# Kernel optimization log

Hardware: AMD Instinct MI355X
Metric: run time of the kernel (lower is better)

The kernel has to match this reference:

```python
import jax, jax.numpy as jnp
import numpy as np

DIM = 1024
HEADS = 16
HEAD_DIM = DIM // HEADS
EPS = 1e-5
THETA = 10000.0


def _rope(t):
    # t: (b, s, d). lucidrains rotary: interleaved pairs, full-dim rotation, theta=10000.
    b, s, d = t.shape
    inv_freq = 1.0 / (THETA ** (jnp.arange(0, d, 2, dtype=jnp.float32) / d))  # (d/2,)
    ang = jnp.arange(s, dtype=jnp.float32)[:, None] * inv_freq[None, :]        # (s, d/2)
    cos, sin = jnp.cos(ang), jnp.sin(ang)
    tp = t.reshape(b, s, d // 2, 2)
    x1, x2 = tp[..., 0], tp[..., 1]
    o1 = x1 * cos - x2 * sin
    o2 = x2 * cos + x1 * sin
    return jnp.stack([o1, o2], axis=-1).reshape(b, s, d)


def setup_inputs() -> dict:
    key = jax.random.key(0)
    ks = jax.random.split(key, 10)
    b, s, d = 2, 2048, DIM
    scale = 1.0 / np.sqrt(d)
    return {
        "x": jax.random.normal(ks[0], (b, s, d), dtype=jnp.float32),
        "mask": jax.random.normal(ks[1], (b, s, s), dtype=jnp.float32),
        "ln_g": jnp.ones((d,), dtype=jnp.float32),
        "ln_b": jnp.zeros((d,), dtype=jnp.float32),
        "w_qkv": jax.random.normal(ks[2], (3 * d, d), dtype=jnp.float32) * scale,
        "b_qkv": jnp.zeros((3 * d,), dtype=jnp.float32),
        "in_w": jax.random.normal(ks[3], (3 * d, d), dtype=jnp.float32) * scale,
        "in_b": jnp.zeros((3 * d,), dtype=jnp.float32),
        "out_w": jax.random.normal(ks[4], (d, d), dtype=jnp.float32) * scale,
        "out_b": jnp.zeros((d,), dtype=jnp.float32),
    }


def reference(x, mask, ln_g, ln_b, w_qkv, b_qkv, in_w, in_b, out_w, out_b):
    b, s, d = x.shape
    # LayerNorm
    mu = jnp.mean(x, axis=-1, keepdims=True)
    var = jnp.mean((x - mu) ** 2, axis=-1, keepdims=True)
    xn = (x - mu) * jax.lax.rsqrt(var + EPS) * ln_g + ln_b
    # fused qkv projection, then chunk
    qkv = xn @ w_qkv.T + b_qkv
    q, k, v = jnp.split(qkv, 3, axis=-1)
    # RoPE on q, k (full dim, interleaved pairs)
    q = _rope(q)
    k = _rope(k)
    # nn.MultiheadAttention re-applies its own in-projection
    wq, wk, wv = jnp.split(in_w, 3, axis=0)
    bq, bk, bv = jnp.split(in_b, 3, axis=0)
    def to_heads(t, w, bias):
        t = t @ w.T + bias
        return t.reshape(b, s, HEADS, HEAD_DIM).transpose(0, 2, 1, 3)  # (b,h,s,hd)
    qh = to_heads(q, wq, bq)
    kh = to_heads(k, wk, bk)
    vh = to_heads(v, wv, bv)
    scores = jnp.einsum('bhid,bhjd->bhij', qh, kh) / np.sqrt(HEAD_DIM)
    scores = scores + mask[:, None, :, :]  # mask repeated over heads
    attn = jax.nn.softmax(scores, axis=-1)
    out = jnp.einsum('bhij,bhjd->bhid', attn, vh)
    out = out.transpose(0, 2, 1, 3).reshape(b, s, d)
    return out @ out_w.T + out_b
```

## Files before the change

### kernel.cpp

```cpp
#include <hip/hip_runtime.h>

using u16 = unsigned short;
using u32 = unsigned int;
typedef __attribute__((ext_vector_type(8))) short short8;
typedef __attribute__((ext_vector_type(4))) float f32x4;

#define LOG2E 1.4426950408889634f
#define SCALE2 0.18033688011112042f

__device__ __forceinline__ u16 f2b(float f) {
  union { float f; unsigned u; } v; v.f = f;
  unsigned r = v.u + 0x7fffu + ((v.u >> 16) & 1u);
  return (u16)(r >> 16);
}

__device__ __forceinline__ void wg_barrier() {
  asm volatile("s_waitcnt lgkmcnt(0)\n\ts_barrier" ::: "memory");
}

__device__ __forceinline__ void gload_lds16(const void* g, void* l) {
  __builtin_amdgcn_global_load_lds(
      (const __attribute__((address_space(1))) unsigned int*)g,
      (__attribute__((address_space(3))) unsigned int*)l, 16, 0, 0);
}

__global__ __launch_bounds__(256) void prep(const float* __restrict__ w_qkv, u16* __restrict__ wqkv_b,
                                            const float* __restrict__ in_w, u16* __restrict__ inw_b,
                                            const float* __restrict__ out_w, u16* __restrict__ outw_b,
                                            float2* __restrict__ rtab,
                                            const float* __restrict__ mask, u16* __restrict__ maskp,
                                            const float* __restrict__ x,
                                            const float* __restrict__ ln_g,
                                            const float* __restrict__ ln_b,
                                            u16* __restrict__ xn) {
  __shared__ u16 T[128 * 68];
  __shared__ float sbuf[4], ssbuf[4];
  int blk = blockIdx.x, t = threadIdx.x;
  if (blk < 7168) {
    int i = blk * 256 + t;
    const float* s; u16* d; int off;
    if (i < 786432)       { s = w_qkv; d = wqkv_b; off = i; }
    else if (i < 1572864) { s = in_w;  d = inw_b;  off = i - 786432; }
    else                  { s = out_w; d = outw_b; off = i - 1572864; }
    float4 v = ((const float4*)s)[off];
    uint2 o;
    o.x = (unsigned)f2b(v.x) | ((unsigned)f2b(v.y) << 16);
    o.y = (unsigned)f2b(v.z) | ((unsigned)f2b(v.w) << 16);
    ((uint2*)d)[off] = o;
  } else if (blk < 11264) {
    int idx = (blk - 7168) * 256 + t;
    int pos = idx >> 9, i = idx & 511;
    float ifreq = exp2f(-(float)(2 * i) * (13.287712379549449f / 1024.0f));
    float ang = (float)pos * ifreq;
    rtab[idx] = make_float2(__cosf(ang), __sinf(ang));
  } else if (blk < 12288) {
    int mb = blk - 11264;
    int kt = mb & 31, qt = (mb >> 5) & 15, bb = mb >> 9;
    const float* src = mask + ((size_t)bb * 2048 + qt * 128) * 2048 + kt * 64;
    #pragma unroll
    for (int it = 0; it < 8; it++) {
      int id = it * 256 + t;
      int r = id >> 4, c4 = (id & 15) * 4;
      float4 v = *(const float4*)(src + (size_t)r * 2048 + c4);
      T[r * 68 + c4 + 0] = f2b(v.x * LOG2E);
      T[r * 68 + c4 + 1] = f2b(v.y * LOG2E);
      T[r * 68 + c4 + 2] = f2b(v.z * LOG2E);
      T[r * 68 + c4 + 3] = f2b(v.w * LOG2E);
    }
    __syncthreads();
    size_t obase = (size_t)(((bb * 16 + qt) * 32) + kt) * 8192;
    #pragma unroll
    for (int it = 0; it < 2; it++) {
      int pos = it * 256 + t;
      int l15 = pos & 15, g = pos >> 4;
      int w = g >> 3, p = (g >> 2) & 1, qd = g & 3;
      int qlocal = w * 32 + p * 16 + l15;
      u16 vals[16];
      #pragma unroll
      for (int mt = 0; mt < 4; mt++)
        #pragma unroll
        for (int reg = 0; reg < 4; reg++)
          vals[mt * 4 + reg] = T[qlocal * 68 + mt * 16 + qd * 4 + reg];
      uint4* dst = (uint4*)(maskp + obase + (size_t)pos * 16);
      dst[0] = *(uint4*)&vals[0];
      dst[1] = *(uint4*)&vals[8];
    }
  } else {
    int row = blk - 12288;
    const float* xr = x + (size_t)row * 1024;
    float4 v = *(const float4*)(xr + t * 4);
    float s = v.x + v.y + v.z + v.w;
    float ss = v.x * v.x + v.y * v.y + v.z * v.z + v.w * v.w;
    #pragma unroll
    for (int m = 1; m < 64; m <<= 1) {
      s  += __shfl_xor(s, m);
      ss += __shfl_xor(ss, m);
    }
    int wave = t >> 6, lane = t & 63;
    if (lane == 0) { sbuf[wave] = s; ssbuf[wave] = ss; }
    __syncthreads();
    s  = sbuf[0] + sbuf[1] + sbuf[2] + sbuf[3];
    ss = ssbuf[0] + ssbuf[1] + ssbuf[2] + ssbuf[3];
    float mean = s * (1.0f / 1024.0f);
    float var  = ss * (1.0f / 1024.0f) - mean * mean;
    float rstd = 1.0f / sqrtf(var + 1e-5f);
    float4 gv = *(const float4*)(ln_g + t * 4);
    float4 bv = *(const float4*)(ln_b + t * 4);
    uint2 o;
    o.x = (unsigned)f2b((v.x - mean) * rstd * gv.x + bv.x) |
          ((unsigned)f2b((v.y - mean) * rstd * gv.y + bv.y) << 16);
    o.y = (unsigned)f2b((v.z - mean) * rstd * gv.z + bv.z) |
          ((unsigned)f2b((v.w - mean) * rstd * gv.w + bv.w) << 16);
    *(uint2*)(xn + (size_t)row * 1024 + t * 4) = o;
  }
}

template<bool SLAB, bool OUT_BF16, bool ROPE, bool WVT>
__global__ __launch_bounds__(256, 3) void gemm_pipe(const u16* __restrict__ A, int lda,
                                                    const u16* __restrict__ W,
                                                    const float* __restrict__ bias,
                                                    const float2* __restrict__ rtab,
                                                    float* __restrict__ Cf,
                                                    u16* __restrict__ Cb,
                                                    u16* __restrict__ vT,
                                                    int ldc, int K) {
  __shared__ u16 As[3][128 * 32];
  __shared__ u16 Bs[3][128 * 32];
  int n0 = blockIdx.x * 128, m0 = blockIdx.y * 128;
  int aoff = SLAB ? ((n0 >> 10) << 10) : 0;
  int tid = threadIdx.x;
  int lane = tid & 63, l15 = lane & 15, quad = lane >> 4;
  int w = tid >> 6, mw = w & 1, nw = w >> 1;
  const u16* Abase = A + (size_t)m0 * lda + aoff;
  const u16* Wbase = W + (size_t)n0 * K;
  f32x4 acc[4][4];
  #pragma unroll
  for (int i = 0; i < 4; i++)
    #pragma unroll
    for (int j = 0; j < 4; j++) acc[i][j] = (f32x4){0.f, 0.f, 0.f, 0.f};

  int rl = lane >> 2;
  int qs = ((lane & 3) ^ ((lane >> 3) & 3)) * 16;
  const char* gA0 = (const char*)(Abase + (size_t)(w * 16 + rl) * lda) + qs;
  const char* gA1 = (const char*)(Abase + (size_t)((w + 4) * 16 + rl) * lda) + qs;
  const char* gB0 = (const char*)(Wbase + (size_t)(w * 16 + rl) * K) + qs;
  const char* gB1 = (const char*)(Wbase + (size_t)((w + 4) * 16 + rl) * K) + qs;
  int p16 = (quad ^ ((l15 >> 1) & 3)) * 8;

  #define ISSUE(bf)                                                           \
    gload_lds16(gA0, &As[bf][(w) * 512]);                                     \
    gload_lds16(gA1, &As[bf][(w + 4) * 512]);                                 \
    gload_lds16(gB0, &Bs[bf][(w) * 512]);                                     \
    gload_lds16(gB1, &Bs[bf][(w + 4) * 512]);                                 \
    gA0 += 64; gA1 += 64; gB0 += 64; gB1 += 64;
  #define WBAR4() asm volatile("s_waitcnt vmcnt(4) lgkmcnt(0)\n\ts_barrier" ::: "memory")
  #define WBAR0() asm volatile("s_waitcnt vmcnt(0) lgkmcnt(0)\n\ts_barrier" ::: "memory")
  #define COMPUTE(bf)                                                         \
    {                                                                         \
      short8 af[4], bfr[4];                                                   \
      _Pragma("unroll")                                                       \
      for (int mt = 0; mt < 4; mt++)                                          \
        af[mt] = *(const short8*)&As[bf][(mw * 64 + mt * 16 + l15) * 32 + p16]; \
      _Pragma("unroll")                                                       \
      for (int nt = 0; nt < 4; nt++)                                          \
        bfr[nt] = *(const short8*)&Bs[bf][(nw * 64 + nt * 16 + l15) * 32 + p16]; \
      _Pragma("unroll")                                                       \
      for (int mt = 0; mt < 4; mt++)                                          \
        _Pragma("unroll")                                                     \
        for (int nt = 0; nt < 4; nt++)                                        \
          acc[mt][nt] = __builtin_amdgcn_mfma_f32_16x16x32_bf16(              \
              af[mt], bfr[nt], acc[mt][nt], 0, 0, 0);                         \
    }

  ISSUE(0);
  ISSUE(1);
  WBAR4();
  #pragma unroll 1
  for (int tt = 0; tt < 10; ++tt) {
    ISSUE(2); COMPUTE(0); WBAR4();
    ISSUE(0); COMPUTE(1); WBAR4();
    ISSUE(1); COMPUTE(2); WBAR4();
  }
  COMPUTE(0); WBAR0();
  COMPUTE(1);
  #undef ISSUE
  #undef WBAR4
  #undef WBAR0
  #undef COMPUTE

  int mb = m0 + mw * 64, nb = n0 + nw * 64;
  float bv[4];
  #pragma unroll
  for (int nt = 0; nt < 4; nt++) bv[nt] = bias[nb + nt * 16 + l15];
  #pragma unroll
  for (int mt = 0; mt < 4; mt++)
    #pragma unroll
    for (int nt = 0; nt < 4; nt++) {
      int col = nb + nt * 16 + l15;
      if (WVT && col >= 2048) {
        int hh = (col - 2048) >> 6, dd = (col - 2048) & 63;
        int row0 = mb + mt * 16 + quad * 4;
        int bbi = row0 >> 11, s0 = row0 & 2047;
        u16 vv[4];
        #pragma unroll
        for (int reg = 0; reg < 4; reg++) vv[reg] = f2b(acc[mt][nt][reg] + bv[nt]);
        *(uint2*)&vT[((size_t)((bbi * 16 + hh) * 64 + dd)) * 2048 + s0] = *(uint2*)vv;
      } else {
        #pragma unroll
        for (int reg = 0; reg < 4; reg++) {
          int row = mb + mt * 16 + quad * 4 + reg;
          float val = acc[mt][nt][reg] + bv[nt];
          if (ROPE && col < 2048) {
            float pr = __shfl_xor(val, 1);
            float2 cs = rtab[(size_t)(row & 2047) * 512 + ((col & 1023) >> 1)];
            val = (col & 1) ? fmaf(val, cs.x, pr * cs.y)
                            : fmaf(val, cs.x, -pr * cs.y);
          }
          if (OUT_BF16) Cb[(size_t)row * ldc + col] = f2b(val);
          else          Cf[(size_t)row * ldc + col] = val;
        }
      }
    }
}

__global__ __launch_bounds__(512, 4) void attn_mfma(const u16* __restrict__ qkv2,
                                                    const u16* __restrict__ vT,
                                                    const u16* __restrict__ maskp,
                                                    u16* __restrict__ attn_out) {
  __shared__ u16 Kb[2][64 * 72];
  __shared__ u16 Vb[2][64 * 72];
  __shared__ u16 Ps[128 * 72];
  __shared__ float lsf[128];
  int h = blockIdx.x, qt = blockIdx.y, bb = blockIdx.z;
  int tid = threadIdx.x;
  int lane = tid & 63, l15 = lane & 15, quad = lane >> 4;
  int w = tid >> 6;
  int wq = w & 3, wk = w >> 2;
  int sr = tid >> 3, sc = (tid & 7) * 8;
  const u16* kslab = qkv2 + ((size_t)bb * 2048) * 3072 + 1024 + h * 64;
  const u16* vslab = vT + ((size_t)((bb * 16 + h) * 64)) * 2048;

  {
    int r = tid >> 2, c0 = (tid & 3) * 16;
    const u16* src = qkv2 + (size_t)(bb * 2048 + qt * 128 + r) * 3072 + h * 64 + c0;
    *(uint4*)&Ps[r * 72 + c0]     = *(const uint4*)src;
    *(uint4*)&Ps[r * 72 + c0 + 8] = *(const uint4*)(src + 8);
  }
  {
    *(uint4*)&Kb[0][sr * 72 + sc] = *(const uint4*)(kslab + (size_t)sr * 3072 + sc);
    *(uint4*)&Vb[0][sr * 72 + sc] = *(const uint4*)(vslab + (size_t)sr * 2048 + sc);
  }
  const u16* mbase = maskp + ((size_t)((bb * 16 + qt) * 32)) * 8192
                     + ((wq * 8 + quad) * 16 + l15) * 16 + wk * 8;
  uint4 m0 = *(const uint4*)mbase;
  uint4 m1 = *(const uint4*)(mbase + 1024);
  wg_barrier();

  short8 bq[2][2];
  #pragma unroll
  for (int p = 0; p < 2; p++)
    #pragma unroll
    for (int hk = 0; hk < 2; hk++)
      bq[p][hk] = *(const short8*)&Ps[(wq * 32 + p * 16 + l15) * 72 + hk * 32 + quad * 8];
  float lsum[2] = {0.f, 0.f};
  f32x4 acc[2][4];
  #pragma unroll
  for (int p = 0; p < 2; p++)
    #pragma unroll
    for (int dt = 0; dt < 4; dt++) acc[p][dt] = (f32x4){0.f, 0.f, 0.f, 0.f};

  for (int kt = 0; kt < 32; kt++) {
    int b = kt & 1;
    uint4 kr, vr, m0n, m1n;
    if (kt + 1 < 32) {
      kr = *(const uint4*)(kslab + (size_t)((kt + 1) * 64 + sr) * 3072 + sc);
      vr = *(const uint4*)(vslab + (size_t)sr * 2048 + (kt + 1) * 64 + sc);
      m0n = *(const uint4*)(mbase + (size_t)(kt + 1) * 8192);
      m1n = *(const uint4*)(mbase + (size_t)(kt + 1) * 8192 + 1024);
    }
    short8 ak[2][2];
    #pragma unroll
    for (int mt = 0; mt < 2; mt++)
      #pragma unroll
      for (int hk = 0; hk < 2; hk++)
        ak[mt][hk] = *(const short8*)&Kb[b][(wk * 32 + mt * 16 + l15) * 72 + hk * 32 + quad * 8];
    f32x4 st[2][2];
    #pragma unroll
    for (int p = 0; p < 2; p++)
      #pragma unroll
      for (int mt = 0; mt < 2; mt++) {
        f32x4 z = (f32x4){0.f, 0.f, 0.f, 0.f};
        z = __builtin_amdgcn_mfma_f32_16x16x32_bf16(ak[mt][0], bq[p][0], z, 0, 0, 0);
        st[p][mt] = __builtin_amdgcn_mfma_f32_16x16x32_bf16(ak[mt][1], bq[p][1], z, 0, 0, 0);
      }
    #pragma unroll
    for (int p = 0; p < 2; p++) {
      uint4 mm = p ? m1 : m0;
      u32 wds[4] = {mm.x, mm.y, mm.z, mm.w};
      float mv[8];
      #pragma unroll
      for (int j = 0; j < 4; j++) {
        mv[2 * j]     = __uint_as_float(wds[j] << 16);
        mv[2 * j + 1] = __uint_as_float(wds[j] & 0xffff0000u);
      }
      int prow = (wq * 32 + p * 16 + l15) * 72 + wk * 32 + quad * 4;
      #pragma unroll
      for (int mt = 0; mt < 2; mt++) {
        float sv0 = fmaf(st[p][mt][0], SCALE2, mv[mt * 4 + 0]);
        float sv1 = fmaf(st[p][mt][1], SCALE2, mv[mt * 4 + 1]);
        float sv2 = fmaf(st[p][mt][2], SCALE2, mv[mt * 4 + 2]);
        float sv3 = fmaf(st[p][mt][3], SCALE2, mv[mt * 4 + 3]);
        float p0 = __builtin_amdgcn_exp2f(sv0), p1 = __builtin_amdgcn_exp2f(sv1);
        float p2 = __builtin_amdgcn_exp2f(sv2), p3 = __builtin_amdgcn_exp2f(sv3);
        lsum[p] += (p0 + p1) + (p2 + p3);
        u32 pk0, pk1;
        asm("v_cvt_pk_bf16_f32 %0, %1, %2" : "=v"(pk0) : "v"(p0), "v"(p1));
        asm("v_cvt_pk_bf16_f32 %0, %1, %2" : "=v"(pk1) : "v"(p2), "v"(p3));
        *(uint2*)&Ps[prow + mt * 16] = make_uint2(pk0, pk1);
      }
    }
    short8 ap[2];
    #pragma unroll
    for (int p = 0; p < 2; p++)
      ap[p] = *(const short8*)&Ps[(wq * 32 + p * 16 + l15) * 72 + wk * 32 + quad * 8];
    #pragma unroll
    for (int dt = 0; dt < 4; dt++) {
      short8 bv = *(const short8*)&Vb[b][(dt * 16 + l15) * 72 + wk * 32 + quad * 8];
      #pragma unroll
      for (int p = 0; p < 2; p++)
        acc[p][dt] = __builtin_amdgcn_mfma_f32_16x16x32_bf16(ap[p], bv, acc[p][dt], 0, 0, 0);
    }
    if (kt + 1 < 32) {
      int nb = b ^ 1;
      *(uint4*)&Kb[nb][sr * 72 + sc] = kr;
      *(uint4*)&Vb[nb][sr * 72 + sc] = vr;
      m0 = m0n; m1 = m1n;
    }
    wg_barrier();
  }

  float* fs = ((wq < 2) ? (float*)&Kb[0][0] : (float*)&Vb[0][0]) + (wq & 1) * 2176;
  if (wk) {
    #pragma unroll
    for (int p = 0; p < 2; p++) {
      #pragma unroll
      for (int dt = 0; dt < 4; dt++)
        #pragma unroll
        for (int reg = 0; reg < 4; reg++)
          fs[(p * 16 + quad * 4 + reg) * 68 + dt * 16 + l15] = acc[p][dt][reg];
      float l = lsum[p];
      l += __shfl_xor(l, 16);
      l += __shfl_xor(l, 32);
      if (lane < 16) lsf[(wq * 2 + p) * 16 + l15] = l;
    }
  }
  wg_barrier();
  if (!wk) {
    #pragma unroll
    for (int p = 0; p < 2; p++) {
      float l = lsum[p];
      l += __shfl_xor(l, 16);
      l += __shfl_xor(l, 32);
      l += lsf[(wq * 2 + p) * 16 + l15];
      #pragma unroll
      for (int reg = 0; reg < 4; reg++) {
        float lq = __shfl(l, quad * 4 + reg);
        float inv = 1.0f / lq;
        int grow = bb * 2048 + qt * 128 + wq * 32 + p * 16 + quad * 4 + reg;
        #pragma unroll
        for (int dt = 0; dt < 4; dt++) {
          float o = acc[p][dt][reg] + fs[(p * 16 + quad * 4 + reg) * 68 + dt * 16 + l15];
          attn_out[(size_t)grow * 1024 + h * 64 + dt * 16 + l15] = f2b(o * inv);
        }
      }
    }
  }
}

extern "C" void kernel_launch(void* const* d_in, const int* in_sizes, int n_in,
                              void* d_out, int out_size, void* d_ws, size_t ws_size,
                              hipStream_t stream) {
  const float* x     = (const float*)d_in[0];
  const float* mask  = (const float*)d_in[1];
  const float* ln_g  = (const float*)d_in[2];
  const float* ln_b  = (const float*)d_in[3];
  const float* w_qkv = (const float*)d_in[4];
  const float* b_qkv = (const float*)d_in[5];
  const float* in_w  = (const float*)d_in[6];
  const float* in_b  = (const float*)d_in[7];
  const float* out_w = (const float*)d_in[8];
  const float* out_b = (const float*)d_in[9];
  float* out = (float*)d_out;
  char* ws = (char*)d_ws;

  u16* wqkv_b = (u16*)(ws);
  u16* inw_b  = (u16*)(ws + 6291456ull);
  u16* outw_b = (u16*)(ws + 12582912ull);
  u16* xn_b   = (u16*)(ws + 14680064ull);
  u16* attn_b = xn_b;
  u16* qkv_b  = (u16*)(ws + 23068672ull);
  u16* qkv2_b = (u16*)(ws + 48234496ull);
  float2* rtab = (float2*)qkv2_b;
  u16* vT     = (u16*)(ws + 73400320ull);
  u16* maskp  = (u16*)(ws + 81788928ull);

  prep<<<16384, 256, 0, stream>>>(w_qkv, wqkv_b, in_w, inw_b, out_w, outw_b,
                                  rtab, mask, maskp, x, ln_g, ln_b, xn_b);
  gemm_pipe<false, true, true, false><<<dim3(24, 32), 256, 0, stream>>>(
      xn_b, 1024, wqkv_b, b_qkv, rtab, nullptr, qkv_b, nullptr, 3072, 1024);
  gemm_pipe<true, true, false, true><<<dim3(24, 32), 256, 0, stream>>>(
      qkv_b, 3072, inw_b, in_b, nullptr, nullptr, qkv2_b, vT, 3072, 1024);
  attn_mfma<<<dim3(16, 16, 2), 512, 0, stream>>>(qkv2_b, vT, maskp, attn_b);
  gemm_pipe<false, false, false, false><<<dim3(8, 32), 256, 0, stream>>>(
      attn_b, 1024, outw_b, out_b, nullptr, out, nullptr, nullptr, 1024, 1024);
}
```

Baseline: 293.4 us.

## Read fp32 mask directly in attention and drop mask pre-conversion pass

Removes the prep stage that converted the fp32 mask to a permuted bf16 layout scaled by log2e. The attention kernel now loads fp32 mask values straight from the input with strided float4 reads, prefetched one key tile ahead, and applies the log2e scale in the softmax FMA. This saves a full read of the mask plus a write of the bf16 copy in prep. In exchange, the attention kernel moves twice the mask bytes per head in a less coalesced pattern, relying on the 16 head blocks that share each mask tile hitting in cache.

```diff
diff --git a/kernel.cpp b/kernel.cpp
--- a/kernel.cpp
+++ b/kernel.cpp
@@ -28,12 +28,10 @@
                                             const float* __restrict__ in_w, u16* __restrict__ inw_b,
                                             const float* __restrict__ out_w, u16* __restrict__ outw_b,
                                             float2* __restrict__ rtab,
-                                            const float* __restrict__ mask, u16* __restrict__ maskp,
                                             const float* __restrict__ x,
                                             const float* __restrict__ ln_g,
                                             const float* __restrict__ ln_b,
                                             u16* __restrict__ xn) {
-  __shared__ u16 T[128 * 68];
   __shared__ float sbuf[4], ssbuf[4];
   int blk = blockIdx.x, t = threadIdx.x;
   if (blk < 7168) {
@@ -53,40 +51,8 @@
     float ifreq = exp2f(-(float)(2 * i) * (13.287712379549449f / 1024.0f));
     float ang = (float)pos * ifreq;
     rtab[idx] = make_float2(__cosf(ang), __sinf(ang));
-  } else if (blk < 12288) {
-    int mb = blk - 11264;
-    int kt = mb & 31, qt = (mb >> 5) & 15, bb = mb >> 9;
-    const float* src = mask + ((size_t)bb * 2048 + qt * 128) * 2048 + kt * 64;
-    #pragma unroll
-    for (int it = 0; it < 8; it++) {
-      int id = it * 256 + t;
-      int r = id >> 4, c4 = (id & 15) * 4;
-      float4 v = *(const float4*)(src + (size_t)r * 2048 + c4);
-      T[r * 68 + c4 + 0] = f2b(v.x * LOG2E);
-      T[r * 68 + c4 + 1] = f2b(v.y * LOG2E);
-      T[r * 68 + c4 + 2] = f2b(v.z * LOG2E);
-      T[r * 68 + c4 + 3] = f2b(v.w * LOG2E);
-    }
-    __syncthreads();
-    size_t obase = (size_t)(((bb * 16 + qt) * 32) + kt) * 8192;
-    #pragma unroll
-    for (int it = 0; it < 2; it++) {
-      int pos = it * 256 + t;
-      int l15 = pos & 15, g = pos >> 4;
-      int w = g >> 3, p = (g >> 2) & 1, qd = g & 3;
-      int qlocal = w * 32 + p * 16 + l15;
-      u16 vals[16];
-      #pragma unroll
-      for (int mt = 0; mt < 4; mt++)
-        #pragma unroll
-        for (int reg = 0; reg < 4; reg++)
-          vals[mt * 4 + reg] = T[qlocal * 68 + mt * 16 + qd * 4 + reg];
-      uint4* dst = (uint4*)(maskp + obase + (size_t)pos * 16);
-      dst[0] = *(uint4*)&vals[0];
-      dst[1] = *(uint4*)&vals[8];
-    }
   } else {
-    int row = blk - 12288;
+    int row = blk - 11264;
     const float* xr = x + (size_t)row * 1024;
     float4 v = *(const float4*)(xr + t * 4);
     float s = v.x + v.y + v.z + v.w;
@@ -225,7 +191,7 @@
 
 __global__ __launch_bounds__(512, 4) void attn_mfma(const u16* __restrict__ qkv2,
                                                     const u16* __restrict__ vT,
-                                                    const u16* __restrict__ maskp,
+                                                    const float* __restrict__ mask,
                                                     u16* __restrict__ attn_out) {
   __shared__ u16 Kb[2][64 * 72];
   __shared__ u16 Vb[2][64 * 72];
@@ -250,10 +216,14 @@
     *(uint4*)&Kb[0][sr * 72 + sc] = *(const uint4*)(kslab + (size_t)sr * 3072 + sc);
     *(uint4*)&Vb[0][sr * 72 + sc] = *(const uint4*)(vslab + (size_t)sr * 2048 + sc);
   }
-  const u16* mbase = maskp + ((size_t)((bb * 16 + qt) * 32)) * 8192
-                     + ((wq * 8 + quad) * 16 + l15) * 16 + wk * 8;
-  uint4 m0 = *(const uint4*)mbase;
-  uint4 m1 = *(const uint4*)(mbase + 1024);
+  const float* mptr = mask + (size_t)(bb * 2048 + qt * 128 + wq * 32 + l15) * 2048
+                      + wk * 32 + quad * 4;
+  float4 mc[2][2];
+  #pragma unroll
+  for (int p = 0; p < 2; p++)
+    #pragma unroll
+    for (int mt = 0; mt < 2; mt++)
+      mc[p][mt] = *(const float4*)(mptr + p * 32768 + mt * 16);
   wg_barrier();
 
   short8 bq[2][2];
@@ -271,12 +241,16 @@
 
   for (int kt = 0; kt < 32; kt++) {
     int b = kt & 1;
-    uint4 kr, vr, m0n, m1n;
+    uint4 kr, vr;
+    float4 mn[2][2];
     if (kt + 1 < 32) {
       kr = *(const uint4*)(kslab + (size_t)((kt + 1) * 64 + sr) * 3072 + sc);
       vr = *(const uint4*)(vslab + (size_t)sr * 2048 + (kt + 1) * 64 + sc);
-      m0n = *(const uint4*)(mbase + (size_t)(kt + 1) * 8192);
-      m1n = *(const uint4*)(mbase + (size_t)(kt + 1) * 8192 + 1024);
+      #pragma unroll
+      for (int p = 0; p < 2; p++)
+        #pragma unroll
+        for (int mt = 0; mt < 2; mt++)
+          mn[p][mt] = *(const float4*)(mptr + (kt + 1) * 64 + p * 32768 + mt * 16);
     }
     short8 ak[2][2];
     #pragma unroll
@@ -295,21 +269,13 @@
       }
     #pragma unroll
     for (int p = 0; p < 2; p++) {
-      uint4 mm = p ? m1 : m0;
-      u32 wds[4] = {mm.x, mm.y, mm.z, mm.w};
-      float mv[8];
-      #pragma unroll
-      for (int j = 0; j < 4; j++) {
-        mv[2 * j]     = __uint_as_float(wds[j] << 16);
-        mv[2 * j + 1] = __uint_as_float(wds[j] & 0xffff0000u);
-      }
       int prow = (wq * 32 + p * 16 + l15) * 72 + wk * 32 + quad * 4;
       #pragma unroll
       for (int mt = 0; mt < 2; mt++) {
-        float sv0 = fmaf(st[p][mt][0], SCALE2, mv[mt * 4 + 0]);
-        float sv1 = fmaf(st[p][mt][1], SCALE2, mv[mt * 4 + 1]);
-        float sv2 = fmaf(st[p][mt][2], SCALE2, mv[mt * 4 + 2]);
-        float sv3 = fmaf(st[p][mt][3], SCALE2, mv[mt * 4 + 3]);
+        float sv0 = fmaf(st[p][mt][0], SCALE2, mc[p][mt].x * LOG2E);
+        float sv1 = fmaf(st[p][mt][1], SCALE2, mc[p][mt].y * LOG2E);
+        float sv2 = fmaf(st[p][mt][2], SCALE2, mc[p][mt].z * LOG2E);
+        float sv3 = fmaf(st[p][mt][3], SCALE2, mc[p][mt].w * LOG2E);
         float p0 = __builtin_amdgcn_exp2f(sv0), p1 = __builtin_amdgcn_exp2f(sv1);
         float p2 = __builtin_amdgcn_exp2f(sv2), p3 = __builtin_amdgcn_exp2f(sv3);
         lsum[p] += (p0 + p1) + (p2 + p3);
@@ -334,7 +300,11 @@
       int nb = b ^ 1;
       *(uint4*)&Kb[nb][sr * 72 + sc] = kr;
       *(uint4*)&Vb[nb][sr * 72 + sc] = vr;
-      m0 = m0n; m1 = m1n;
+      #pragma unroll
+      for (int p = 0; p < 2; p++)
+        #pragma unroll
+        for (int mt = 0; mt < 2; mt++)
+          mc[p][mt] = mn[p][mt];
     }
     wg_barrier();
   }
@@ -402,15 +372,14 @@
   u16* qkv2_b = (u16*)(ws + 48234496ull);
   float2* rtab = (float2*)qkv2_b;
   u16* vT     = (u16*)(ws + 73400320ull);
-  u16* maskp  = (u16*)(ws + 81788928ull);
-
-  prep<<<16384, 256, 0, stream>>>(w_qkv, wqkv_b, in_w, inw_b, out_w, outw_b,
-                                  rtab, mask, maskp, x, ln_g, ln_b, xn_b);
+
+  prep<<<15360, 256, 0, stream>>>(w_qkv, wqkv_b, in_w, inw_b, out_w, outw_b,
+                                  rtab, x, ln_g, ln_b, xn_b);
   gemm_pipe<false, true, true, false><<<dim3(24, 32), 256, 0, stream>>>(
       xn_b, 1024, wqkv_b, b_qkv, rtab, nullptr, qkv_b, nullptr, 3072, 1024);
   gemm_pipe<true, true, false, true><<<dim3(24, 32), 256, 0, stream>>>(
       qkv_b, 3072, inw_b, in_b, nullptr, nullptr, qkv2_b, vT, 3072, 1024);
-  attn_mfma<<<dim3(16, 16, 2), 512, 0, stream>>>(qkv2_b, vT, maskp, attn_b);
+  attn_mfma<<<dim3(16, 16, 2), 512, 0, stream>>>(qkv2_b, vT, mask, attn_b);
   gemm_pipe<false, false, false, false><<<dim3(8, 32), 256, 0, stream>>>(
       attn_b, 1024, outw_b, out_b, nullptr, out, nullptr, nullptr, 1024, 1024);
 }
```

After: 306.2 us. 4.4% more time.
